# Kernel optimization log

Hardware: AMD Instinct MI355X
Metric: run time of the kernel (lower is better)

Reference implementation:

```python
import jax, jax.numpy as jnp
import numpy as np

B, D, U, M, K = 8192, 512, 512, 16, 64


def setup_inputs() -> dict:
    key = jax.random.key(0)
    ks = jax.random.split(key, 5)
    return {
        "x": jax.random.normal(ks[0], (B, D), dtype=jnp.float32),
        "key_kernel": jax.random.normal(ks[1], (D, K), dtype=jnp.float32) * (1.0 / np.sqrt(D)),
        "key_bias": jnp.zeros((K,), dtype=jnp.float32),
        "keys_map": jax.random.normal(ks[2], (M, K), dtype=jnp.float32),
        "kernels": jax.random.normal(ks[3], (M, D, U), dtype=jnp.float32) * (1.0 / np.sqrt(D)),
        "biases": jnp.zeros((M, U), dtype=jnp.float32),
    }


def reference(x, key_kernel, key_bias, keys_map, kernels, biases):
    # key projection: [B, K]
    keyv = x @ key_kernel + key_bias
    # inverse-distance similarity to mode keys: [B, M]
    dist = jnp.sqrt(jnp.sum((keyv[:, None, :] - keys_map[None, :, :]) ** 2, axis=-1))
    sim = 1.0 / (dist + 1.0)
    modes = kernels.shape[0]
    # kernel = mean_m(sim_m * kernels_m); out = x @ kernel.
    # Distributive identity: out = (1/M) * sum_m sim_m * (x @ kernels_m)
    out = jnp.einsum("bm,bd,mdu->bu", sim, x, kernels) / modes
    # bias = mean_m(sim_m * biases_m): [B, U]
    out = out + (sim @ biases) / modes
    return out
```

## Files before the change

kernel.cpp:

```cpp
#include <hip/hip_runtime.h>
#include <hip/hip_bf16.h>
#include <stdint.h>

#define B_SZ 8192
#define D_SZ 512
#define U_SZ 512
#define M_SZ 16
#define K_SZ 64

typedef short bf16x8 __attribute__((ext_vector_type(8)));
typedef float f32x4 __attribute__((ext_vector_type(4)));

__device__ __forceinline__ unsigned short f2bf(float f) {
  union { float f; unsigned u; } v; v.f = f;
  unsigned r = v.u + 0x7fffu + ((v.u >> 16) & 1u);
  return (unsigned short)(r >> 16);
}

__global__ __launch_bounds__(256) void prep1(
    const float* __restrict__ x, const float* __restrict__ key_kernel,
    const float* __restrict__ kernels, unsigned short* __restrict__ xbf,
    unsigned short* __restrict__ kbf, unsigned short* __restrict__ wkbf) {
  __shared__ float tf[32][65];
  __shared__ unsigned short sx[16][520];
  int bid = blockIdx.x;
  int t = threadIdx.x;

  if (bid < 2048) {
    int m = bid >> 7;
    int rem = bid & 127;
    int a = (rem >> 3) & 15;
    int ut = rem & 7;
    int d0 = a * 32, u0 = ut * 64;
    {
      int dr = t >> 4, uc = t & 15;
      const float* src = kernels + ((size_t)m * D_SZ + d0 + dr) * U_SZ + u0 + uc * 4;
      float4 aa = *(const float4*)src;
      float4 bb = *(const float4*)(src + (size_t)16 * U_SZ);
      tf[dr][uc * 4 + 0] = aa.x; tf[dr][uc * 4 + 1] = aa.y;
      tf[dr][uc * 4 + 2] = aa.z; tf[dr][uc * 4 + 3] = aa.w;
      tf[dr + 16][uc * 4 + 0] = bb.x; tf[dr + 16][uc * 4 + 1] = bb.y;
      tf[dr + 16][uc * 4 + 2] = bb.z; tf[dr + 16][uc * 4 + 3] = bb.w;
    }
    __syncthreads();
    {
      int j = t >> 6;
      int lp = t & 63;
      int dc = lp >> 4, lane16 = lp & 15;
      int kt = a >> 1, h = a & 1;
      int ur = j * 16 + lane16;
      unsigned short* dst = kbf +
          (((((size_t)m * 8 + ut) * 8 + kt) * 4 + j) * 2 + h) * 512 +
          (size_t)lp * 8;
      ushort4 lo, hi;
      lo.x = f2bf(tf[dc * 8 + 0][ur]); lo.y = f2bf(tf[dc * 8 + 1][ur]);
      lo.z = f2bf(tf[dc * 8 + 2][ur]); lo.w = f2bf(tf[dc * 8 + 3][ur]);
      hi.x = f2bf(tf[dc * 8 + 4][ur]); hi.y = f2bf(tf[dc * 8 + 5][ur]);
      hi.z = f2bf(tf[dc * 8 + 6][ur]); hi.w = f2bf(tf[dc * 8 + 7][ur]);
      *(ushort4*)dst = lo;
      *(ushort4*)(dst + 4) = hi;
    }
    return;
  }

  if (bid < 2056) {
    int kt = bid - 2048;
#pragma unroll
    for (int rep = 0; rep < 2; ++rep) {
      int c = rep * 256 + t;
      int j = c >> 7, h = (c >> 6) & 1, quad = (c >> 4) & 3, ln = c & 15;
      int dd = kt * 64 + h * 32 + quad * 8;
      int u = j * 16 + ln;
      unsigned short v[8];
#pragma unroll
      for (int e = 0; e < 8; ++e)
        v[e] = f2bf(key_kernel[(size_t)(dd + e) * K_SZ + u]);
      unsigned short* dst =
          wkbf + ((size_t)((kt * 4 + j) * 2 + h) * 64 + quad * 16 + ln) * 8;
#pragma unroll
      for (int e = 0; e < 8; ++e) dst[e] = v[e];
    }
    return;
  }

  {
    int xb0 = bid - 2056;
    int btx = xb0 >> 3, i = xb0 & 7;
    int b0 = xb0 * 16;
#pragma unroll
    for (int rep = 0; rep < 8; ++rep) {
      int idx = rep * 256 + t;
      int row = idx >> 7;
      int c4 = (idx & 127) * 4;
      float4 v = *(const float4*)(x + (size_t)(b0 + row) * D_SZ + c4);
      ushort4 o;
      o.x = f2bf(v.x); o.y = f2bf(v.y); o.z = f2bf(v.z); o.w = f2bf(v.w);
      *(ushort4*)(&sx[row][c4]) = o;
    }
    __syncthreads();
    int w = t >> 6, l = t & 63;
    int ln = l & 15, quad = l >> 4;
#pragma unroll
    for (int rep = 0; rep < 4; ++rep) {
      int c = w * 4 + rep;
      int kt = c >> 1, h = c & 1;
      const unsigned short* srcp = &sx[ln][kt * 64 + h * 32 + quad * 8];
      ushort4 lo = *(const ushort4*)(srcp);
      ushort4 hi = *(const ushort4*)(srcp + 4);
      unsigned short* dst =
          xbf + ((((size_t)btx * 8 + kt) * 8 + i) * 2 + h) * 512 + (size_t)l * 8;
      *(ushort4*)dst = lo;
      *(ushort4*)(dst + 4) = hi;
    }
  }
}

#define GLL(src_, dst_)                                                        \
  __builtin_amdgcn_global_load_lds(                                            \
      (const __attribute__((address_space(1))) unsigned int*)(src_),           \
      (__attribute__((address_space(3))) unsigned int*)(dst_), 16, 0, 0)

#define STAGE(mode_, kt_, bufi_)                                               \
  {                                                                            \
    const unsigned short* _src = kbf_l +                                       \
        (((size_t)(mode_) * 8 + ut) * 8 + (kt_)) * 4096 + w * 512;             \
    unsigned short* _dst = Bbuf + (bufi_) * 4096 + w * 512;                    \
    GLL(_src, _dst);                                                           \
  }

#define LOAD_AF(dst_, kt_)                                                     \
  _Pragma("unroll") for (int ii = 0; ii < 2; ++ii)                             \
      _Pragma("unroll") for (int h = 0; h < 2; ++h) {                          \
    int g_ = bt * 16 + w * 2 + ii;                                             \
    dst_[ii][h] = *(const bf16x8*)(                                            \
        xbf + ((((size_t)(g_ >> 3) * 8 + (kt_)) * 8 + (g_ & 7)) * 2 + h) *     \
                  512 +                                                        \
              (size_t)l * 8);                                                  \
  }

__global__ __launch_bounds__(512, 2) void poly_gemm(
    const unsigned short* __restrict__ xbf,
    const unsigned short* __restrict__ kbf,
    const unsigned short* __restrict__ wkbf,
    const float* __restrict__ key_bias,
    const float* __restrict__ keys_map,
    const float* __restrict__ biases,
    float* __restrict__ out) {
  __shared__ __align__(16) char smem[94208];

  int t = threadIdx.x, w = t >> 6, l = t & 63;
  int bid = blockIdx.x;
  int ut = bid & 7, bt = bid >> 3;
  int b0 = bt * 256, u0 = ut * 64;
  int lane16 = l & 15, quad = l >> 4;

  unsigned short* Bbuf = (unsigned short*)smem;
  float* kvp = (float*)smem;
  float* sSim = (float*)(smem + 69632);
  float* sBias = (float*)(smem + 86016);
  float* sKM = (float*)(smem + 90112);

  {
    int bi = t * 2;
    *(float2*)(sBias + bi) =
        *(const float2*)(biases + (size_t)(bi >> 6) * U_SZ + u0 + (bi & 63));
    if (t < 256) ((float4*)sKM)[t] = ((const float4*)keys_map)[t];
  }

  {
    f32x4 kacc[2][4];
#pragma unroll
    for (int ii = 0; ii < 2; ++ii)
#pragma unroll
      for (int j = 0; j < 4; ++j) kacc[ii][j] = (f32x4){0.f, 0.f, 0.f, 0.f};
    for (int kt = 0; kt < 8; ++kt) {
      bf16x8 a2[2][2];
      LOAD_AF(a2, kt);
#pragma unroll
      for (int j = 0; j < 4; ++j) {
        bf16x8 w0 = *(const bf16x8*)(wkbf + ((size_t)((kt * 4 + j) * 2 + 0) * 64 + l) * 8);
        bf16x8 w1 = *(const bf16x8*)(wkbf + ((size_t)((kt * 4 + j) * 2 + 1) * 64 + l) * 8);
#pragma unroll
        for (int ii = 0; ii < 2; ++ii) {
          kacc[ii][j] = __builtin_amdgcn_mfma_f32_16x16x32_bf16(a2[ii][0], w0, kacc[ii][j], 0, 0, 0);
          kacc[ii][j] = __builtin_amdgcn_mfma_f32_16x16x32_bf16(a2[ii][1], w1, kacc[ii][j], 0, 0, 0);
        }
      }
    }
#pragma unroll
    for (int j = 0; j < 4; ++j) {
      float bc = key_bias[j * 16 + lane16];
#pragma unroll
      for (int ii = 0; ii < 2; ++ii)
#pragma unroll
        for (int r = 0; r < 4; ++r)
          kvp[(size_t)(w * 32 + ii * 16 + quad * 4 + r) * 68 + j * 16 + lane16] =
              kacc[ii][j][r] + bc;
    }
  }
  __syncthreads();

  {
    int row = t >> 1, mg = (t & 1) * 8;
    float d2[8] = {0.f, 0.f, 0.f, 0.f, 0.f, 0.f, 0.f, 0.f};
#pragma unroll 8
    for (int k = 0; k < 64; ++k) {
      float kvv = kvp[(size_t)row * 68 + k];
#pragma unroll
      for (int q = 0; q < 8; ++q) {
        float df = kvv - sKM[(mg + q) * 64 + k];
        d2[q] += df * df;
      }
    }
#pragma unroll
    for (int q = 0; q < 8; ++q)
      sSim[(mg + q) * 256 + row] = 1.0f / (sqrtf(d2[q]) + 1.0f);
  }
  __syncthreads();

  const unsigned short* kbf_l = kbf + (size_t)l * 8;
  bf16x8 afc[2][2], afn[2][2];
  STAGE(0, 0, 0);
  STAGE(1, 0, 1);
  STAGE(2, 0, 2);
  STAGE(3, 0, 3);
  LOAD_AF(afc, 0);
  asm volatile("s_waitcnt vmcnt(0)" ::: "memory");
  __syncthreads();

  f32x4 facc[2][4];
#pragma unroll
  for (int i = 0; i < 2; ++i)
#pragma unroll
    for (int j = 0; j < 4; ++j) facc[i][j] = (f32x4){0.f, 0.f, 0.f, 0.f};

#pragma unroll 1
  for (int kt = 0; kt < 8; ++kt) {
#pragma unroll
    for (int mode = 0; mode < 16; ++mode) {
      const int s = kt * 16 + mode;
      {
        int mode4 = (mode + 4) & 15;
        int kt4 = (mode >= 12) ? ((kt + 1) & 7) : kt;
        STAGE(mode4, kt4, (s + 4) & 7);
      }
      if (mode == 0 && kt < 7) { LOAD_AF(afn, kt + 1); }
      if (mode < 5) {
        if (kt < 7)
          asm volatile("s_waitcnt vmcnt(8)" ::: "memory");
        else
          asm volatile("s_waitcnt vmcnt(4)" ::: "memory");
      } else {
        asm volatile("s_waitcnt vmcnt(4)" ::: "memory");
      }
      asm volatile("s_barrier" ::: "memory");

      const unsigned short* lb = Bbuf + (s & 7) * 4096;
      bf16x8 bfr[4][2];
#pragma unroll
      for (int j = 0; j < 4; ++j)
#pragma unroll
        for (int h = 0; h < 2; ++h)
          bfr[j][h] = *(const bf16x8*)(lb + (j * 2 + h) * 512 + (size_t)l * 8);

      f32x4 sv[2];
#pragma unroll
      for (int i = 0; i < 2; ++i)
        sv[i] =
            *(const f32x4*)(sSim + mode * 256 + w * 32 + i * 16 + quad * 4);

#pragma unroll
      for (int i = 0; i < 2; ++i)
#pragma unroll
        for (int j = 0; j < 4; ++j) {
          f32x4 p = __builtin_amdgcn_mfma_f32_16x16x32_bf16(
              afc[i][0], bfr[j][0], (f32x4){0.f, 0.f, 0.f, 0.f}, 0, 0, 0);
          p = __builtin_amdgcn_mfma_f32_16x16x32_bf16(afc[i][1], bfr[j][1], p,
                                                      0, 0, 0);
#pragma unroll
          for (int r = 0; r < 4; ++r) facc[i][j][r] += sv[i][r] * p[r];
        }

      if (kt == 0) {
        float bbv[4];
#pragma unroll
        for (int j = 0; j < 4; ++j)
          bbv[j] = sBias[mode * 64 + j * 16 + lane16];
#pragma unroll
        for (int i = 0; i < 2; ++i)
#pragma unroll
          for (int j = 0; j < 4; ++j)
#pragma unroll
            for (int r = 0; r < 4; ++r) facc[i][j][r] += sv[i][r] * bbv[j];
      }
    }
    if (kt < 7) {
#pragma unroll
      for (int ii = 0; ii < 2; ++ii)
#pragma unroll
        for (int h = 0; h < 2; ++h) afc[ii][h] = afn[ii][h];
    }
  }

  asm volatile("s_waitcnt vmcnt(0)" ::: "memory");
#pragma unroll
  for (int i = 0; i < 2; ++i)
#pragma unroll
    for (int r = 0; r < 4; ++r) {
      int row = b0 + w * 32 + i * 16 + quad * 4 + r;
      float* orow = out + (size_t)row * U_SZ + u0;
#pragma unroll
      for (int j = 0; j < 4; ++j)
        orow[j * 16 + lane16] = facc[i][j][r] * 0.0625f;
    }
}

extern "C" void kernel_launch(void* const* d_in, const int* in_sizes, int n_in,
                              void* d_out, int out_size, void* d_ws, size_t ws_size,
                              hipStream_t stream) {
  const float* x = (const float*)d_in[0];
  const float* key_kernel = (const float*)d_in[1];
  const float* key_bias = (const float*)d_in[2];
  const float* keys_map = (const float*)d_in[3];
  const float* kernels = (const float*)d_in[4];
  const float* biases = (const float*)d_in[5];
  float* out = (float*)d_out;

  char* p = (char*)d_ws;
  unsigned short* xbf = (unsigned short*)p;  p += (size_t)B_SZ * D_SZ * 2;
  unsigned short* kbf = (unsigned short*)p;  p += (size_t)M_SZ * U_SZ * D_SZ * 2;
  unsigned short* wkbf = (unsigned short*)p;

  prep1<<<dim3(2568), 256, 0, stream>>>(x, key_kernel, kernels, xbf, kbf, wkbf);
  poly_gemm<<<dim3(256), 512, 0, stream>>>(xbf, kbf, wkbf, key_bias, keys_map,
                                           biases, out);
}
```

Before: 170.6 us.

## Fuse prep and GEMM into one cooperative kernel with grid sync

Merges the bf16 conversion/relayout kernel into the main GEMM kernel as a cooperative launch. Each of the 256 blocks converts its share of kernels, x and key_kernel, then a grid-wide sync precedes the main work. The first B-tile stages are issued before the key projection so their loads overlap it, and the kvp buffer is moved to a separate LDS region with stride 65. This removes a kernel launch boundary and the tail of the prep kernel. In exchange it needs 153 KB of LDS per block, which likely limits occupancy to one block per CU, and it adds the cost of a grid barrier.

```diff
diff --git a/kernel.cpp b/kernel.cpp
--- a/kernel.cpp
+++ b/kernel.cpp
@@ -1,6 +1,9 @@
 #include <hip/hip_runtime.h>
+#include <hip/hip_cooperative_groups.h>
 #include <hip/hip_bf16.h>
 #include <stdint.h>
+
+namespace cg = cooperative_groups;
 
 #define B_SZ 8192
 #define D_SZ 512
@@ -15,104 +18,6 @@
   union { float f; unsigned u; } v; v.f = f;
   unsigned r = v.u + 0x7fffu + ((v.u >> 16) & 1u);
   return (unsigned short)(r >> 16);
-}
-
-__global__ __launch_bounds__(256) void prep1(
-    const float* __restrict__ x, const float* __restrict__ key_kernel,
-    const float* __restrict__ kernels, unsigned short* __restrict__ xbf,
-    unsigned short* __restrict__ kbf, unsigned short* __restrict__ wkbf) {
-  __shared__ float tf[32][65];
-  __shared__ unsigned short sx[16][520];
-  int bid = blockIdx.x;
-  int t = threadIdx.x;
-
-  if (bid < 2048) {
-    int m = bid >> 7;
-    int rem = bid & 127;
-    int a = (rem >> 3) & 15;
-    int ut = rem & 7;
-    int d0 = a * 32, u0 = ut * 64;
-    {
-      int dr = t >> 4, uc = t & 15;
-      const float* src = kernels + ((size_t)m * D_SZ + d0 + dr) * U_SZ + u0 + uc * 4;
-      float4 aa = *(const float4*)src;
-      float4 bb = *(const float4*)(src + (size_t)16 * U_SZ);
-      tf[dr][uc * 4 + 0] = aa.x; tf[dr][uc * 4 + 1] = aa.y;
-      tf[dr][uc * 4 + 2] = aa.z; tf[dr][uc * 4 + 3] = aa.w;
-      tf[dr + 16][uc * 4 + 0] = bb.x; tf[dr + 16][uc * 4 + 1] = bb.y;
-      tf[dr + 16][uc * 4 + 2] = bb.z; tf[dr + 16][uc * 4 + 3] = bb.w;
-    }
-    __syncthreads();
-    {
-      int j = t >> 6;
-      int lp = t & 63;
-      int dc = lp >> 4, lane16 = lp & 15;
-      int kt = a >> 1, h = a & 1;
-      int ur = j * 16 + lane16;
-      unsigned short* dst = kbf +
-          (((((size_t)m * 8 + ut) * 8 + kt) * 4 + j) * 2 + h) * 512 +
-          (size_t)lp * 8;
-      ushort4 lo, hi;
-      lo.x = f2bf(tf[dc * 8 + 0][ur]); lo.y = f2bf(tf[dc * 8 + 1][ur]);
-      lo.z = f2bf(tf[dc * 8 + 2][ur]); lo.w = f2bf(tf[dc * 8 + 3][ur]);
-      hi.x = f2bf(tf[dc * 8 + 4][ur]); hi.y = f2bf(tf[dc * 8 + 5][ur]);
-      hi.z = f2bf(tf[dc * 8 + 6][ur]); hi.w = f2bf(tf[dc * 8 + 7][ur]);
-      *(ushort4*)dst = lo;
-      *(ushort4*)(dst + 4) = hi;
-    }
-    return;
-  }
-
-  if (bid < 2056) {
-    int kt = bid - 2048;
-#pragma unroll
-    for (int rep = 0; rep < 2; ++rep) {
-      int c = rep * 256 + t;
-      int j = c >> 7, h = (c >> 6) & 1, quad = (c >> 4) & 3, ln = c & 15;
-      int dd = kt * 64 + h * 32 + quad * 8;
-      int u = j * 16 + ln;
-      unsigned short v[8];
-#pragma unroll
-      for (int e = 0; e < 8; ++e)
-        v[e] = f2bf(key_kernel[(size_t)(dd + e) * K_SZ + u]);
-      unsigned short* dst =
-          wkbf + ((size_t)((kt * 4 + j) * 2 + h) * 64 + quad * 16 + ln) * 8;
-#pragma unroll
-      for (int e = 0; e < 8; ++e) dst[e] = v[e];
-    }
-    return;
-  }
-
-  {
-    int xb0 = bid - 2056;
-    int btx = xb0 >> 3, i = xb0 & 7;
-    int b0 = xb0 * 16;
-#pragma unroll
-    for (int rep = 0; rep < 8; ++rep) {
-      int idx = rep * 256 + t;
-      int row = idx >> 7;
-      int c4 = (idx & 127) * 4;
-      float4 v = *(const float4*)(x + (size_t)(b0 + row) * D_SZ + c4);
-      ushort4 o;
-      o.x = f2bf(v.x); o.y = f2bf(v.y); o.z = f2bf(v.z); o.w = f2bf(v.w);
-      *(ushort4*)(&sx[row][c4]) = o;
-    }
-    __syncthreads();
-    int w = t >> 6, l = t & 63;
-    int ln = l & 15, quad = l >> 4;
-#pragma unroll
-    for (int rep = 0; rep < 4; ++rep) {
-      int c = w * 4 + rep;
-      int kt = c >> 1, h = c & 1;
-      const unsigned short* srcp = &sx[ln][kt * 64 + h * 32 + quad * 8];
-      ushort4 lo = *(const ushort4*)(srcp);
-      ushort4 hi = *(const ushort4*)(srcp + 4);
-      unsigned short* dst =
-          xbf + ((((size_t)btx * 8 + kt) * 8 + i) * 2 + h) * 512 + (size_t)l * 8;
-      *(ushort4*)dst = lo;
-      *(ushort4*)(dst + 4) = hi;
-    }
-  }
 }
 
 #define GLL(src_, dst_)                                                        \
@@ -138,15 +43,13 @@
               (size_t)l * 8);                                                  \
   }
 
-__global__ __launch_bounds__(512, 2) void poly_gemm(
-    const unsigned short* __restrict__ xbf,
-    const unsigned short* __restrict__ kbf,
-    const unsigned short* __restrict__ wkbf,
-    const float* __restrict__ key_bias,
-    const float* __restrict__ keys_map,
-    const float* __restrict__ biases,
-    float* __restrict__ out) {
-  __shared__ __align__(16) char smem[94208];
+__global__ __launch_bounds__(512, 2) void poly_fused(
+    const float* __restrict__ x, const float* __restrict__ key_kernel,
+    const float* __restrict__ key_bias, const float* __restrict__ keys_map,
+    const float* __restrict__ kernels, const float* __restrict__ biases,
+    unsigned short* __restrict__ xbf, unsigned short* __restrict__ kbf,
+    unsigned short* __restrict__ wkbf, float* __restrict__ out) {
+  __shared__ __align__(16) char smem[156672];
 
   int t = threadIdx.x, w = t >> 6, l = t & 63;
   int bid = blockIdx.x;
@@ -155,10 +58,107 @@
   int lane16 = l & 15, quad = l >> 4;
 
   unsigned short* Bbuf = (unsigned short*)smem;
-  float* kvp = (float*)smem;
-  float* sSim = (float*)(smem + 69632);
-  float* sBias = (float*)(smem + 86016);
-  float* sKM = (float*)(smem + 90112);
+  float* kvp = (float*)(smem + 65536);
+  float* sSim = (float*)(smem + 132096);
+  float* sBias = (float*)(smem + 148480);
+  float* sKM = (float*)(smem + 152576);
+
+  float(*tf2)[32][65] = (float(*)[32][65])smem;
+  unsigned short(*sx2)[16][520] =
+      (unsigned short(*)[16][520])(smem + 16640);
+
+  {
+    int th = t & 255, hs = t >> 8;
+
+#pragma unroll 1
+    for (int rep = 0; rep < 4; ++rep) {
+      int task = bid * 8 + rep * 2 + hs;
+      int m = task >> 7;
+      int rem = task & 127;
+      int a = (rem >> 3) & 15;
+      int utt = rem & 7;
+      int d0 = a * 32;
+      {
+        int dr = th >> 4, uc = th & 15;
+        const float* src =
+            kernels + ((size_t)m * D_SZ + d0 + dr) * U_SZ + utt * 64 + uc * 4;
+        float4 aa = *(const float4*)src;
+        float4 bb = *(const float4*)(src + (size_t)16 * U_SZ);
+        tf2[hs][dr][uc * 4 + 0] = aa.x; tf2[hs][dr][uc * 4 + 1] = aa.y;
+        tf2[hs][dr][uc * 4 + 2] = aa.z; tf2[hs][dr][uc * 4 + 3] = aa.w;
+        tf2[hs][dr + 16][uc * 4 + 0] = bb.x; tf2[hs][dr + 16][uc * 4 + 1] = bb.y;
+        tf2[hs][dr + 16][uc * 4 + 2] = bb.z; tf2[hs][dr + 16][uc * 4 + 3] = bb.w;
+      }
+      __syncthreads();
+      {
+        int j = th >> 6, lp = th & 63;
+        int dc = lp >> 4, l16 = lp & 15;
+        int kt0 = a >> 1, h = a & 1;
+        int ur = j * 16 + l16;
+        unsigned short* dst = kbf +
+            (((((size_t)m * 8 + utt) * 8 + kt0) * 4 + j) * 2 + h) * 512 +
+            (size_t)lp * 8;
+        ushort4 lo, hi;
+        lo.x = f2bf(tf2[hs][dc * 8 + 0][ur]); lo.y = f2bf(tf2[hs][dc * 8 + 1][ur]);
+        lo.z = f2bf(tf2[hs][dc * 8 + 2][ur]); lo.w = f2bf(tf2[hs][dc * 8 + 3][ur]);
+        hi.x = f2bf(tf2[hs][dc * 8 + 4][ur]); hi.y = f2bf(tf2[hs][dc * 8 + 5][ur]);
+        hi.z = f2bf(tf2[hs][dc * 8 + 6][ur]); hi.w = f2bf(tf2[hs][dc * 8 + 7][ur]);
+        *(ushort4*)dst = lo;
+        *(ushort4*)(dst + 4) = hi;
+      }
+      __syncthreads();
+    }
+
+    {
+      int task = bid * 2 + hs;
+      int btx = task >> 3, i = task & 7;
+      int b0x = task * 16;
+#pragma unroll
+      for (int rep = 0; rep < 8; ++rep) {
+        int idx = rep * 256 + th;
+        int row = idx >> 7;
+        int c4 = (idx & 127) * 4;
+        float4 v = *(const float4*)(x + (size_t)(b0x + row) * D_SZ + c4);
+        ushort4 o;
+        o.x = f2bf(v.x); o.y = f2bf(v.y); o.z = f2bf(v.z); o.w = f2bf(v.w);
+        *(ushort4*)(&sx2[hs][row][c4]) = o;
+      }
+      __syncthreads();
+      int w2 = th >> 6, lx = th & 63;
+      int ln = lx & 15, qx = lx >> 4;
+#pragma unroll
+      for (int rep = 0; rep < 4; ++rep) {
+        int c = w2 * 4 + rep;
+        int ktx = c >> 1, hx = c & 1;
+        const unsigned short* srcp = &sx2[hs][ln][ktx * 64 + hx * 32 + qx * 8];
+        ushort4 lo = *(const ushort4*)(srcp);
+        ushort4 hi = *(const ushort4*)(srcp + 4);
+        unsigned short* dst = xbf +
+            ((((size_t)btx * 8 + ktx) * 8 + i) * 2 + hx) * 512 + (size_t)lx * 8;
+        *(ushort4*)dst = lo;
+        *(ushort4*)(dst + 4) = hi;
+      }
+    }
+
+    if (bid < 8) {
+      int ktw = bid;
+      int c = t;
+      int j = c >> 7, h = (c >> 6) & 1, qw = (c >> 4) & 3, ln = c & 15;
+      int dd = ktw * 64 + h * 32 + qw * 8;
+      int u = j * 16 + ln;
+      unsigned short v[8];
+#pragma unroll
+      for (int e = 0; e < 8; ++e)
+        v[e] = f2bf(key_kernel[(size_t)(dd + e) * K_SZ + u]);
+      unsigned short* dst =
+          wkbf + ((size_t)((ktw * 4 + j) * 2 + h) * 64 + qw * 16 + ln) * 8;
+#pragma unroll
+      for (int e = 0; e < 8; ++e) dst[e] = v[e];
+    }
+  }
+
+  __threadfence();
+  cg::this_grid().sync();
 
   {
     int bi = t * 2;
@@ -167,6 +167,12 @@
     if (t < 256) ((float4*)sKM)[t] = ((const float4*)keys_map)[t];
   }
 
+  const unsigned short* kbf_l = kbf + (size_t)l * 8;
+  STAGE(0, 0, 0);
+  STAGE(1, 0, 1);
+  STAGE(2, 0, 2);
+  STAGE(3, 0, 3);
+
   {
     f32x4 kacc[2][4];
 #pragma unroll
@@ -194,7 +200,7 @@
       for (int ii = 0; ii < 2; ++ii)
 #pragma unroll
         for (int r = 0; r < 4; ++r)
-          kvp[(size_t)(w * 32 + ii * 16 + quad * 4 + r) * 68 + j * 16 + lane16] =
+          kvp[(size_t)(w * 32 + ii * 16 + quad * 4 + r) * 65 + j * 16 + lane16] =
               kacc[ii][j][r] + bc;
     }
   }
@@ -205,7 +211,7 @@
     float d2[8] = {0.f, 0.f, 0.f, 0.f, 0.f, 0.f, 0.f, 0.f};
 #pragma unroll 8
     for (int k = 0; k < 64; ++k) {
-      float kvv = kvp[(size_t)row * 68 + k];
+      float kvv = kvp[(size_t)row * 65 + k];
 #pragma unroll
       for (int q = 0; q < 8; ++q) {
         float df = kvv - sKM[(mg + q) * 64 + k];
@@ -216,14 +222,8 @@
     for (int q = 0; q < 8; ++q)
       sSim[(mg + q) * 256 + row] = 1.0f / (sqrtf(d2[q]) + 1.0f);
   }
-  __syncthreads();
-
-  const unsigned short* kbf_l = kbf + (size_t)l * 8;
+
   bf16x8 afc[2][2], afn[2][2];
-  STAGE(0, 0, 0);
-  STAGE(1, 0, 1);
-  STAGE(2, 0, 2);
-  STAGE(3, 0, 3);
   LOAD_AF(afc, 0);
   asm volatile("s_waitcnt vmcnt(0)" ::: "memory");
   __syncthreads();
@@ -331,7 +331,10 @@
   unsigned short* kbf = (unsigned short*)p;  p += (size_t)M_SZ * U_SZ * D_SZ * 2;
   unsigned short* wkbf = (unsigned short*)p;
 
-  prep1<<<dim3(2568), 256, 0, stream>>>(x, key_kernel, kernels, xbf, kbf, wkbf);
-  poly_gemm<<<dim3(256), 512, 0, stream>>>(xbf, kbf, wkbf, key_bias, keys_map,
-                                           biases, out);
+  void* kargs[] = {(void*)&x,       (void*)&key_kernel, (void*)&key_bias,
+                   (void*)&keys_map, (void*)&kernels,    (void*)&biases,
+                   (void*)&xbf,     (void*)&kbf,        (void*)&wkbf,
+                   (void*)&out};
+  hipLaunchCooperativeKernel((const void*)poly_fused, dim3(256), dim3(512),
+                             kargs, 0, stream);
 }
```

Result: slower. 274.8 us (+61.1%).
